# Kernel optimization log

Hardware: AMD Instinct MI355X
Metric: run time of the kernel (lower is better)

## Reference

```python
import jax, jax.numpy as jnp
import numpy as np

B, T, D, L = 16, 4096, 512, 1024

def setup_inputs() -> dict:
    key = jax.random.key(0)
    k1, k2, k3, k4 = jax.random.split(key, 4)
    x = jax.random.normal(k1, (B, T, D), dtype=jnp.float32)
    q = jax.random.normal(k2, (L, D), dtype=jnp.float32)
    fc_w = jax.random.normal(k3, (1, D), dtype=jnp.float32) * (1.0 / np.sqrt(D))
    fc_b = jax.random.normal(k4, (1,), dtype=jnp.float32) * 0.01
    return {"x": x, "q": q, "fc_w": fc_w, "fc_b": fc_b}

def reference(x, q, fc_w, fc_b):
    # att: (B, T, L) label-wise attention scores, softmax over sequence axis T
    att = jnp.einsum('btd,ld->btl', x, q)
    att = jax.nn.softmax(att, axis=1)
    # out: (B, L, D) attention-pooled features per label
    out = jnp.einsum('btl,btd->bld', att, x)
    # linear head to scalar per label -> (B, L)
    return jnp.einsum('bld,od->blo', out, fc_w).squeeze(-1) + fc_b[0]
```

## Files before the change

### kernel.cpp

```cpp
#include <hip/hip_runtime.h>

#define B_ 16
#define T_ 4096
#define D_ 512
#define L_ 1024
#define NTCH (T_ / 64)

typedef _Float16 half8 __attribute__((ext_vector_type(8)));
typedef float float4v __attribute__((ext_vector_type(4)));

__device__ inline void gl_lds(const void* g, void* l) {
    __builtin_amdgcn_global_load_lds(
        (const __attribute__((address_space(1))) unsigned int*)g,
        (__attribute__((address_space(3))) unsigned int*)l, 16, 0, 0);
}

__global__ __launch_bounds__(256) void k_y(const float* __restrict__ x,
                                           const float* __restrict__ w,
                                           float* __restrict__ y) {
    int row  = (blockIdx.x * 256 + threadIdx.x) >> 6;
    int lane = threadIdx.x & 63;
    const float* r = x + (size_t)row * D_;
    float s = 0.f;
#pragma unroll
    for (int k = 0; k < D_; k += 64) s = fmaf(r[k + lane], w[k + lane], s);
#pragma unroll
    for (int o = 32; o > 0; o >>= 1) s += __shfl_xor(s, o, 64);
    if (lane == 0) y[row] = s;
}

__global__ __launch_bounds__(256) void k_cvt(const float* __restrict__ src,
                                             _Float16* __restrict__ dst) {
    int idx = blockIdx.x * 256 + threadIdx.x;
    int g   = idx & 63;
    int row = idx >> 6;
    const float* p = src + (size_t)row * D_ + g * 8;
    float4 a = *(const float4*)p;
    float4 c = *(const float4*)(p + 4);
    half8 h;
    h[0] = (_Float16)a.x; h[1] = (_Float16)a.y; h[2] = (_Float16)a.z; h[3] = (_Float16)a.w;
    h[4] = (_Float16)c.x; h[5] = (_Float16)c.y; h[6] = (_Float16)c.z; h[7] = (_Float16)c.w;
    size_t blk = (size_t)(row >> 4) * (D_ / 32) + (g >> 2);
    ((half8*)dst)[blk * 64 + (row & 15) + 16 * (g & 3)] = h;
}

__global__ __launch_bounds__(256, 2) void k_mfma(const _Float16* __restrict__ xt,
                                                 const _Float16* __restrict__ qt,
                                                 const float* __restrict__ y,
                                                 float* __restrict__ part) {
    __shared__ half8 S[1024];
    __shared__ float ys[128];

    const int tid  = threadIdx.x;
    const int lane = tid & 63;
    const int w    = tid >> 6;
    const int b    = blockIdx.z;
    const int tb0  = b * (T_ / 16) + blockIdx.y * 8;
    const int lb0  = blockIdx.x * 8;

    if (tid < 128) ys[tid] = y[(size_t)b * T_ + blockIdx.y * 128 + tid];

    float4v acc[4][4];
#pragma unroll
    for (int i = 0; i < 4; ++i)
#pragma unroll
        for (int j = 0; j < 4; ++j) acc[i][j] = (float4v){0.f, 0.f, 0.f, 0.f};

    const half8* Xg = (const half8*)xt;
    const half8* Qg = (const half8*)qt;
    const int xa = tb0 + 2 * w;
    const int qa = lb0 + 2 * w;
    const int ts = (w >> 1) * 4, ls = (w & 1) * 4;

    for (int kc = 0; kc < D_ / 32; ++kc) {
        __syncthreads();
        gl_lds(Xg + ((size_t)xa * (D_ / 32) + kc) * 64 + lane,       &S[(2 * w) * 64]);
        gl_lds(Xg + ((size_t)(xa + 1) * (D_ / 32) + kc) * 64 + lane, &S[(2 * w + 1) * 64]);
        gl_lds(Qg + ((size_t)qa * (D_ / 32) + kc) * 64 + lane,       &S[512 + (2 * w) * 64]);
        gl_lds(Qg + ((size_t)(qa + 1) * (D_ / 32) + kc) * 64 + lane, &S[512 + (2 * w + 1) * 64]);
        __syncthreads();

        half8 A[4], Bv[4];
#pragma unroll
        for (int i = 0; i < 4; ++i) A[i] = S[(ts + i) * 64 + lane];
#pragma unroll
        for (int j = 0; j < 4; ++j) Bv[j] = S[512 + (ls + j) * 64 + lane];
#pragma unroll
        for (int i = 0; i < 4; ++i)
#pragma unroll
            for (int j = 0; j < 4; ++j)
                acc[i][j] = __builtin_amdgcn_mfma_f32_16x16x32_f16(A[i], Bv[j], acc[i][j], 0, 0, 0);
    }

    const int quad = lane >> 4, cl = lane & 15;
    const int tw = (w >> 1) * 64;
    const int tchunk = blockIdx.y * 2 + (w >> 1);
    const int lbase = blockIdx.x * 128 + (w & 1) * 64;

#pragma unroll
    for (int j = 0; j < 4; ++j) {
        float m = -1e30f;
#pragma unroll
        for (int i = 0; i < 4; ++i)
#pragma unroll
            for (int r = 0; r < 4; ++r) m = fmaxf(m, acc[i][j][r]);
        float z = 0.f, n = 0.f;
#pragma unroll
        for (int i = 0; i < 4; ++i)
#pragma unroll
            for (int r = 0; r < 4; ++r) {
                float p = __expf(acc[i][j][r] - m);
                z += p;
                n = fmaf(p, ys[tw + i * 16 + quad * 4 + r], n);
            }
#pragma unroll
        for (int msk = 16; msk <= 32; msk <<= 1) {
            float om = __shfl_xor(m, msk, 64);
            float oz = __shfl_xor(z, msk, 64);
            float on = __shfl_xor(n, msk, 64);
            float mn = fmaxf(m, om);
            float s0 = __expf(m - mn), s1 = __expf(om - mn);
            z = fmaf(z, s0, oz * s1);
            n = fmaf(n, s0, on * s1);
            m = mn;
        }
        if (quad == 0) {
            int l = lbase + j * 16 + cl;
            size_t idx = ((size_t)(b * L_ + l) * NTCH + tchunk) * 3;
            part[idx + 0] = m;
            part[idx + 1] = z;
            part[idx + 2] = n;
        }
    }
}

#define NC 8
#define TC (T_ / NC)
#define BT 128
#define BL 128
#define KK 32

__global__ __launch_bounds__(256, 2) void k_main(const float* __restrict__ x,
                                                 const float* __restrict__ q,
                                                 const float* __restrict__ y,
                                                 float* __restrict__ part) {
    __shared__ float Xs[KK][BT + 4];
    __shared__ float Qs[KK][BL + 4];
    const int tid = threadIdx.x;
    const int ty = tid & 15, tx = tid >> 4;
    const int lb = blockIdx.x * BL, chunk = blockIdx.y, b = blockIdx.z;
    const int g = tid & 7, r0 = tid >> 3;

    float run_m[8], run_z[8], run_n[8];
#pragma unroll
    for (int j = 0; j < 8; ++j) { run_m[j] = -1e30f; run_z[j] = 0.f; run_n[j] = 0.f; }

    for (int tt = 0; tt < TC; tt += BT) {
        const int t0 = chunk * TC + tt;
        float s[8][8];
#pragma unroll
        for (int i = 0; i < 8; ++i)
#pragma unroll
            for (int j = 0; j < 8; ++j) s[i][j] = 0.f;
        for (int kc = 0; kc < D_; kc += KK) {
            __syncthreads();
#pragma unroll
            for (int p = 0; p < 4; ++p) {
                int rr = p * 32 + r0;
                float4 vx = *(const float4*)(x + ((size_t)b * T_ + t0 + rr) * D_ + kc + g * 4);
                float4 vq = *(const float4*)(q + (size_t)(lb + rr) * D_ + kc + g * 4);
                Xs[g * 4 + 0][rr] = vx.x; Xs[g * 4 + 1][rr] = vx.y;
                Xs[g * 4 + 2][rr] = vx.z; Xs[g * 4 + 3][rr] = vx.w;
                Qs[g * 4 + 0][rr] = vq.x; Qs[g * 4 + 1][rr] = vq.y;
                Qs[g * 4 + 2][rr] = vq.z; Qs[g * 4 + 3][rr] = vq.w;
            }
            __syncthreads();
#pragma unroll
            for (int k = 0; k < KK; ++k) {
                float4 a0 = *(const float4*)&Xs[k][ty * 4];
                float4 a1 = *(const float4*)&Xs[k][64 + ty * 4];
                float4 b0 = *(const float4*)&Qs[k][tx * 4];
                float4 b1 = *(const float4*)&Qs[k][64 + tx * 4];
                float av[8] = {a0.x, a0.y, a0.z, a0.w, a1.x, a1.y, a1.z, a1.w};
                float bv[8] = {b0.x, b0.y, b0.z, b0.w, b1.x, b1.y, b1.z, b1.w};
#pragma unroll
                for (int i = 0; i < 8; ++i)
#pragma unroll
                    for (int j = 0; j < 8; ++j) s[i][j] = fmaf(av[i], bv[j], s[i][j]);
            }
        }
        float yv[8];
#pragma unroll
        for (int i = 0; i < 8; ++i) {
            int tl = (i < 4) ? (ty * 4 + i) : (64 + ty * 4 + (i - 4));
            yv[i] = y[(size_t)b * T_ + t0 + tl];
        }
#pragma unroll
        for (int j = 0; j < 8; ++j) {
            float mt = s[0][j];
#pragma unroll
            for (int i = 1; i < 8; ++i) mt = fmaxf(mt, s[i][j]);
            float mn = fmaxf(run_m[j], mt);
            float sc = __expf(run_m[j] - mn);
            float z = run_z[j] * sc, n = run_n[j] * sc;
#pragma unroll
            for (int i = 0; i < 8; ++i) {
                float p = __expf(s[i][j] - mn);
                z += p;
                n = fmaf(p, yv[i], n);
            }
            run_m[j] = mn; run_z[j] = z; run_n[j] = n;
        }
    }
#pragma unroll
    for (int msk = 1; msk < 16; msk <<= 1) {
#pragma unroll
        for (int j = 0; j < 8; ++j) {
            float om = __shfl_xor(run_m[j], msk, 64);
            float oz = __shfl_xor(run_z[j], msk, 64);
            float on = __shfl_xor(run_n[j], msk, 64);
            float mn = fmaxf(run_m[j], om);
            float s0 = __expf(run_m[j] - mn), s1 = __expf(om - mn);
            run_z[j] = fmaf(run_z[j], s0, oz * s1);
            run_n[j] = fmaf(run_n[j], s0, on * s1);
            run_m[j] = mn;
        }
    }
    if (ty == 0) {
#pragma unroll
        for (int j = 0; j < 8; ++j) {
            int ll = (j < 4) ? (tx * 4 + j) : (64 + tx * 4 + (j - 4));
            size_t idx = ((size_t)(b * L_ + lb + ll) * NC + chunk) * 3;
            part[idx + 0] = run_m[j];
            part[idx + 1] = run_z[j];
            part[idx + 2] = run_n[j];
        }
    }
}

__global__ __launch_bounds__(256) void k_comb(const float* __restrict__ part,
                                              const float* __restrict__ fc_b,
                                              float* __restrict__ out, int nc) {
    int bl = blockIdx.x * 256 + threadIdx.x;
    float m = -1e30f, z = 0.f, n = 0.f;
    for (int c = 0; c < nc; ++c) {
        size_t idx = ((size_t)bl * nc + c) * 3;
        float pm = part[idx + 0], pz = part[idx + 1], pn = part[idx + 2];
        float mn = fmaxf(m, pm);
        float s0 = __expf(m - mn), s1 = __expf(pm - mn);
        z = fmaf(z, s0, pz * s1);
        n = fmaf(n, s0, pn * s1);
        m = mn;
    }
    out[bl] = n / z + fc_b[0];
}

extern "C" void kernel_launch(void* const* d_in, const int* in_sizes, int n_in,
                              void* d_out, int out_size, void* d_ws, size_t ws_size,
                              hipStream_t stream) {
    const float* x    = (const float*)d_in[0];
    const float* q    = (const float*)d_in[1];
    const float* fc_w = (const float*)d_in[2];
    const float* fc_b = (const float*)d_in[3];
    float* out = (float*)d_out;
    float* ws  = (float*)d_ws;

    const size_t Y_F    = (size_t)B_ * T_;
    const size_t PART_F = (size_t)B_ * L_ * NTCH * 3;
    const size_t XT_H   = (size_t)B_ * T_ * D_;
    const size_t QT_H   = (size_t)L_ * D_;
    const size_t need   = (Y_F + PART_F) * 4 + (XT_H + QT_H) * 2;

    if (ws_size >= need) {
        float* y    = ws;
        float* part = ws + Y_F;
        _Float16* xt = (_Float16*)(ws + Y_F + PART_F);
        _Float16* qt = xt + XT_H;
        k_y  <<<B_ * T_ / 4, 256, 0, stream>>>(x, fc_w, y);
        k_cvt<<<(B_ * T_ * 64) / 256, 256, 0, stream>>>(x, xt);
        k_cvt<<<(L_ * 64) / 256, 256, 0, stream>>>(q, qt);
        k_mfma<<<dim3(L_ / 128, T_ / 128, B_), 256, 0, stream>>>(xt, qt, y, part);
        k_comb<<<B_ * L_ / 256, 256, 0, stream>>>(part, fc_b, out, NTCH);
    } else {
        float* y    = ws;
        float* part = ws + Y_F;
        k_y   <<<B_ * T_ / 4, 256, 0, stream>>>(x, fc_w, y);
        k_main<<<dim3(L_ / BL, NC, B_), 256, 0, stream>>>(x, q, y, part);
        k_comb<<<B_ * L_ / 256, 256, 0, stream>>>(part, fc_b, out, NC);
    }
}
```

Before: 325.4 us.

## Fuse projection and fp16 conversion into one pass; remap MFMA grid for XCD locality

Merges the fc_w projection kernel and the x fp16 conversion into a single k_prep kernel that stages 16 rows in LDS, so x (128 MB fp32) is read from HBM once instead of twice. The MFMA kernel moves to a flat 1D grid whose block index is decoded so consecutive blocks on the same XCD share a (batch, T-tile) and walk the L tiles, improving L2 reuse of the x tile. It also raises launch_bounds occupancy to 4 blocks per CU, which may force register spilling given the 64-float accumulator.

```diff
diff --git a/kernel.cpp b/kernel.cpp
--- a/kernel.cpp
+++ b/kernel.cpp
@@ -27,6 +27,53 @@
 #pragma unroll
     for (int o = 32; o > 0; o >>= 1) s += __shfl_xor(s, o, 64);
     if (lane == 0) y[row] = s;
+}
+
+__global__ __launch_bounds__(256) void k_prep(const float* __restrict__ x,
+                                              const float* __restrict__ w,
+                                              _Float16* __restrict__ xt,
+                                              float* __restrict__ y) {
+    __shared__ float Xl[16 * 512];
+    __shared__ float wl[512];
+    const int tid = threadIdx.x;
+    const size_t base = (size_t)blockIdx.x * (16 * 512);
+
+    if (tid < 128) ((float4*)wl)[tid] = ((const float4*)w)[tid];
+#pragma unroll
+    for (int it = 0; it < 8; ++it) {
+        int f = it * 1024 + tid * 4;
+        ((float4*)Xl)[f >> 2] = *(const float4*)(x + base + f);
+    }
+    __syncthreads();
+
+    {
+        int row = tid >> 4, seg = tid & 15;
+        float p = 0.f;
+#pragma unroll
+        for (int j = 0; j < 32; ++j) {
+            int k = seg * 32 + ((j + tid) & 31);
+            p = fmaf(Xl[row * 512 + k], wl[k], p);
+        }
+        p += __shfl_xor(p, 1, 64); p += __shfl_xor(p, 2, 64);
+        p += __shfl_xor(p, 4, 64); p += __shfl_xor(p, 8, 64);
+        if (seg == 0) y[blockIdx.x * 16 + row] = p;
+    }
+
+    {
+        int idx = tid & 63, row = idx & 15, gq = idx >> 4;
+        half8* dst = (half8*)xt + (size_t)blockIdx.x * (D_ / 32) * 64;
+#pragma unroll
+        for (int it2 = 0; it2 < 4; ++it2) {
+            int kc = it2 * 4 + (tid >> 6);
+            int k0 = kc * 32 + gq * 8;
+            float4 a = *(float4*)&Xl[row * 512 + k0];
+            float4 c = *(float4*)&Xl[row * 512 + k0 + 4];
+            half8 h;
+            h[0] = (_Float16)a.x; h[1] = (_Float16)a.y; h[2] = (_Float16)a.z; h[3] = (_Float16)a.w;
+            h[4] = (_Float16)c.x; h[5] = (_Float16)c.y; h[6] = (_Float16)c.z; h[7] = (_Float16)c.w;
+            dst[kc * 64 + idx] = h;
+        }
+    }
 }
 
 __global__ __launch_bounds__(256) void k_cvt(const float* __restrict__ src,
@@ -44,21 +91,28 @@
     ((half8*)dst)[blk * 64 + (row & 15) + 16 * (g & 3)] = h;
 }
 
-__global__ __launch_bounds__(256, 2) void k_mfma(const _Float16* __restrict__ xt,
+__global__ __launch_bounds__(256, 4) void k_mfma(const _Float16* __restrict__ xt,
                                                  const _Float16* __restrict__ qt,
                                                  const float* __restrict__ y,
                                                  float* __restrict__ part) {
     __shared__ half8 S[1024];
     __shared__ float ys[128];
 
+    const int bid  = blockIdx.x;
+    const int xcd  = bid & 7;
+    const int jj   = bid >> 3;
+    const int tile = (xcd << 6) | (jj >> 3);
+    const int lblk = jj & 7;
+    const int tblk = tile & 31;
+    const int b    = tile >> 5;
+
     const int tid  = threadIdx.x;
     const int lane = tid & 63;
     const int w    = tid >> 6;
-    const int b    = blockIdx.z;
-    const int tb0  = b * (T_ / 16) + blockIdx.y * 8;
-    const int lb0  = blockIdx.x * 8;
-
-    if (tid < 128) ys[tid] = y[(size_t)b * T_ + blockIdx.y * 128 + tid];
+    const int tb0  = b * (T_ / 16) + tblk * 8;
+    const int lb0  = lblk * 8;
+
+    if (tid < 128) ys[tid] = y[(size_t)b * T_ + tblk * 128 + tid];
 
     float4v acc[4][4];
 #pragma unroll
@@ -94,8 +148,8 @@
 
     const int quad = lane >> 4, cl = lane & 15;
     const int tw = (w >> 1) * 64;
-    const int tchunk = blockIdx.y * 2 + (w >> 1);
-    const int lbase = blockIdx.x * 128 + (w & 1) * 64;
+    const int tchunk = tblk * 2 + (w >> 1);
+    const int lbase = lblk * 128 + (w & 1) * 64;
 
 #pragma unroll
     for (int j = 0; j < 4; ++j) {
@@ -276,10 +330,9 @@
         float* part = ws + Y_F;
         _Float16* xt = (_Float16*)(ws + Y_F + PART_F);
         _Float16* qt = xt + XT_H;
-        k_y  <<<B_ * T_ / 4, 256, 0, stream>>>(x, fc_w, y);
-        k_cvt<<<(B_ * T_ * 64) / 256, 256, 0, stream>>>(x, xt);
-        k_cvt<<<(L_ * 64) / 256, 256, 0, stream>>>(q, qt);
-        k_mfma<<<dim3(L_ / 128, T_ / 128, B_), 256, 0, stream>>>(xt, qt, y, part);
+        k_prep<<<B_ * T_ / 16, 256, 0, stream>>>(x, fc_w, xt, y);
+        k_cvt <<<(L_ * 64) / 256, 256, 0, stream>>>(q, qt);
+        k_mfma<<<4096, 256, 0, stream>>>(xt, qt, y, part);
         k_comb<<<B_ * L_ / 256, 256, 0, stream>>>(part, fc_b, out, NTCH);
     } else {
         float* y    = ws;
```

Result: faster. 301.5 us (-7.3%).

## Fuse fp16 conversion with fc dot-product, remap MFMA grid per XCD, planar partials

Applied to the files above, without the earlier changes.

Merges the separate y = x·fc_w reduction and the fp16 layout conversion into one prep kernel, so x is read once instead of twice. The MFMA kernel moves to a 1D grid with an XCD-aware block mapping that keeps tiles of the same batch on the same XCD to improve L2 reuse, and its launch-bounds occupancy hint rises from 2 to 4. Partial softmax stats are stored as separate planes indexed by L contiguously, so the combine kernel reads coalesced. Occupancy 4 may force register spills given 64 accumulator floats per thread.

```diff
diff --git a/kernel.cpp b/kernel.cpp
--- a/kernel.cpp
+++ b/kernel.cpp
@@ -5,6 +5,7 @@
 #define D_ 512
 #define L_ 1024
 #define NTCH (T_ / 64)
+#define PPLANE ((size_t)B_ * NTCH * L_)
 
 typedef _Float16 half8 __attribute__((ext_vector_type(8)));
 typedef float float4v __attribute__((ext_vector_type(4)));
@@ -15,50 +16,70 @@
         (__attribute__((address_space(3))) unsigned int*)l, 16, 0, 0);
 }
 
-__global__ __launch_bounds__(256) void k_y(const float* __restrict__ x,
-                                           const float* __restrict__ w,
-                                           float* __restrict__ y) {
-    int row  = (blockIdx.x * 256 + threadIdx.x) >> 6;
-    int lane = threadIdx.x & 63;
-    const float* r = x + (size_t)row * D_;
-    float s = 0.f;
-#pragma unroll
-    for (int k = 0; k < D_; k += 64) s = fmaf(r[k + lane], w[k + lane], s);
-#pragma unroll
-    for (int o = 32; o > 0; o >>= 1) s += __shfl_xor(s, o, 64);
-    if (lane == 0) y[row] = s;
-}
-
-__global__ __launch_bounds__(256) void k_cvt(const float* __restrict__ src,
-                                             _Float16* __restrict__ dst) {
-    int idx = blockIdx.x * 256 + threadIdx.x;
-    int g   = idx & 63;
-    int row = idx >> 6;
-    const float* p = src + (size_t)row * D_ + g * 8;
-    float4 a = *(const float4*)p;
-    float4 c = *(const float4*)(p + 4);
-    half8 h;
-    h[0] = (_Float16)a.x; h[1] = (_Float16)a.y; h[2] = (_Float16)a.z; h[3] = (_Float16)a.w;
-    h[4] = (_Float16)c.x; h[5] = (_Float16)c.y; h[6] = (_Float16)c.z; h[7] = (_Float16)c.w;
-    size_t blk = (size_t)(row >> 4) * (D_ / 32) + (g >> 2);
-    ((half8*)dst)[blk * 64 + (row & 15) + 16 * (g & 3)] = h;
-}
-
-__global__ __launch_bounds__(256, 2) void k_mfma(const _Float16* __restrict__ xt,
+__global__ __launch_bounds__(256) void k_prep(const float* __restrict__ src,
+                                              const float* __restrict__ w,
+                                              _Float16* __restrict__ dst,
+                                              float* __restrict__ y, int do_y) {
+    __shared__ float Yp[64];
+    const int tid  = threadIdx.x;
+    const int wv   = tid >> 6;
+    const int lane = tid & 63;
+    const int row  = lane & 15, gq = lane >> 4;
+    const float* bsrc = src + (size_t)blockIdx.x * (16 * 512);
+    half8* bdst = (half8*)dst + (size_t)blockIdx.x * 1024;
+
+    float acc = 0.f;
+#pragma unroll
+    for (int it = 0; it < 4; ++it) {
+        int kc = it * 4 + wv;
+        int k0 = kc * 32 + gq * 8;
+        float4 a = *(const float4*)(bsrc + row * 512 + k0);
+        float4 c = *(const float4*)(bsrc + row * 512 + k0 + 4);
+        half8 h;
+        h[0] = (_Float16)a.x; h[1] = (_Float16)a.y; h[2] = (_Float16)a.z; h[3] = (_Float16)a.w;
+        h[4] = (_Float16)c.x; h[5] = (_Float16)c.y; h[6] = (_Float16)c.z; h[7] = (_Float16)c.w;
+        bdst[kc * 64 + lane] = h;
+        if (do_y) {
+            float4 wa = *(const float4*)(w + k0);
+            float4 wc = *(const float4*)(w + k0 + 4);
+            acc = fmaf(a.x, wa.x, acc); acc = fmaf(a.y, wa.y, acc);
+            acc = fmaf(a.z, wa.z, acc); acc = fmaf(a.w, wa.w, acc);
+            acc = fmaf(c.x, wc.x, acc); acc = fmaf(c.y, wc.y, acc);
+            acc = fmaf(c.z, wc.z, acc); acc = fmaf(c.w, wc.w, acc);
+        }
+    }
+    if (do_y) {
+        acc += __shfl_xor(acc, 16, 64);
+        acc += __shfl_xor(acc, 32, 64);
+        if (gq == 0) Yp[wv * 16 + row] = acc;
+        __syncthreads();
+        if (tid < 16)
+            y[blockIdx.x * 16 + tid] = Yp[tid] + Yp[16 + tid] + Yp[32 + tid] + Yp[48 + tid];
+    }
+}
+
+__global__ __launch_bounds__(256, 4) void k_mfma(const _Float16* __restrict__ xt,
                                                  const _Float16* __restrict__ qt,
                                                  const float* __restrict__ y,
                                                  float* __restrict__ part) {
     __shared__ half8 S[1024];
     __shared__ float ys[128];
 
+    const int bid  = blockIdx.x;
+    const int xcd  = bid & 7;
+    const int jj   = bid >> 3;
+    const int tile = (xcd << 6) | (jj >> 3);
+    const int lblk = jj & 7;
+    const int tblk = tile & 31;
+    const int b    = tile >> 5;
+
     const int tid  = threadIdx.x;
     const int lane = tid & 63;
     const int w    = tid >> 6;
-    const int b    = blockIdx.z;
-    const int tb0  = b * (T_ / 16) + blockIdx.y * 8;
-    const int lb0  = blockIdx.x * 8;
-
-    if (tid < 128) ys[tid] = y[(size_t)b * T_ + blockIdx.y * 128 + tid];
+    const int tb0  = b * (T_ / 16) + tblk * 8;
+    const int lb0  = lblk * 8;
+
+    if (tid < 128) ys[tid] = y[(size_t)b * T_ + tblk * 128 + tid];
 
     float4v acc[4][4];
 #pragma unroll
@@ -94,8 +115,12 @@
 
     const int quad = lane >> 4, cl = lane & 15;
     const int tw = (w >> 1) * 64;
-    const int tchunk = blockIdx.y * 2 + (w >> 1);
-    const int lbase = blockIdx.x * 128 + (w & 1) * 64;
+    const int tchunk = tblk * 2 + (w >> 1);
+    const int lbase = lblk * 128 + (w & 1) * 64;
+
+    float* pm = part;
+    float* pz = part + PPLANE;
+    float* pn = part + 2 * PPLANE;
 
 #pragma unroll
     for (int j = 0; j < 4; ++j) {
@@ -126,12 +151,33 @@
         }
         if (quad == 0) {
             int l = lbase + j * 16 + cl;
-            size_t idx = ((size_t)(b * L_ + l) * NTCH + tchunk) * 3;
-            part[idx + 0] = m;
-            part[idx + 1] = z;
-            part[idx + 2] = n;
-        }
-    }
+            size_t a = ((size_t)b * NTCH + tchunk) * L_ + l;
+            pm[a] = m;
+            pz[a] = z;
+            pn[a] = n;
+        }
+    }
+}
+
+__global__ __launch_bounds__(256) void k_comb_p(const float* __restrict__ part,
+                                                const float* __restrict__ fc_b,
+                                                float* __restrict__ out) {
+    int bl = blockIdx.x * 256 + threadIdx.x;
+    int b = bl >> 10, l = bl & (L_ - 1);
+    const float* pm = part;
+    const float* pz = part + PPLANE;
+    const float* pn = part + 2 * PPLANE;
+    float m = -1e30f, z = 0.f, n = 0.f;
+    for (int c = 0; c < NTCH; ++c) {
+        size_t a = ((size_t)b * NTCH + c) * L_ + l;
+        float pmv = pm[a], pzv = pz[a], pnv = pn[a];
+        float mn = fmaxf(m, pmv);
+        float s0 = __expf(m - mn), s1 = __expf(pmv - mn);
+        z = fmaf(z, s0, pzv * s1);
+        n = fmaf(n, s0, pnv * s1);
+        m = mn;
+    }
+    out[bl] = n / z + fc_b[0];
 }
 
 #define NC 8
@@ -139,6 +185,20 @@
 #define BT 128
 #define BL 128
 #define KK 32
+
+__global__ __launch_bounds__(256) void k_y(const float* __restrict__ x,
+                                           const float* __restrict__ w,
+                                           float* __restrict__ y) {
+    int row  = (blockIdx.x * 256 + threadIdx.x) >> 6;
+    int lane = threadIdx.x & 63;
+    const float* r = x + (size_t)row * D_;
+    float s = 0.f;
+#pragma unroll
+    for (int k = 0; k < D_; k += 64) s = fmaf(r[k + lane], w[k + lane], s);
+#pragma unroll
+    for (int o = 32; o > 0; o >>= 1) s += __shfl_xor(s, o, 64);
+    if (lane == 0) y[row] = s;
+}
 
 __global__ __launch_bounds__(256, 2) void k_main(const float* __restrict__ x,
                                                  const float* __restrict__ q,
@@ -238,13 +298,13 @@
     }
 }
 
-__global__ __launch_bounds__(256) void k_comb(const float* __restrict__ part,
-                                              const float* __restrict__ fc_b,
-                                              float* __restrict__ out, int nc) {
+__global__ __launch_bounds__(256) void k_comb_f(const float* __restrict__ part,
+                                                const float* __restrict__ fc_b,
+                                                float* __restrict__ out) {
     int bl = blockIdx.x * 256 + threadIdx.x;
     float m = -1e30f, z = 0.f, n = 0.f;
-    for (int c = 0; c < nc; ++c) {
-        size_t idx = ((size_t)bl * nc + c) * 3;
+    for (int c = 0; c < NC; ++c) {
+        size_t idx = ((size_t)bl * NC + c) * 3;
         float pm = part[idx + 0], pz = part[idx + 1], pn = part[idx + 2];
         float mn = fmaxf(m, pm);
         float s0 = __expf(m - mn), s1 = __expf(pm - mn);
@@ -266,7 +326,7 @@
     float* ws  = (float*)d_ws;
 
     const size_t Y_F    = (size_t)B_ * T_;
-    const size_t PART_F = (size_t)B_ * L_ * NTCH * 3;
+    const size_t PART_F = 3 * PPLANE;
     const size_t XT_H   = (size_t)B_ * T_ * D_;
     const size_t QT_H   = (size_t)L_ * D_;
     const size_t need   = (Y_F + PART_F) * 4 + (XT_H + QT_H) * 2;
@@ -276,16 +336,15 @@
         float* part = ws + Y_F;
         _Float16* xt = (_Float16*)(ws + Y_F + PART_F);
         _Float16* qt = xt + XT_H;
-        k_y  <<<B_ * T_ / 4, 256, 0, stream>>>(x, fc_w, y);
-        k_cvt<<<(B_ * T_ * 64) / 256, 256, 0, stream>>>(x, xt);
-        k_cvt<<<(L_ * 64) / 256, 256, 0, stream>>>(q, qt);
-        k_mfma<<<dim3(L_ / 128, T_ / 128, B_), 256, 0, stream>>>(xt, qt, y, part);
-        k_comb<<<B_ * L_ / 256, 256, 0, stream>>>(part, fc_b, out, NTCH);
+        k_prep<<<B_ * T_ / 16, 256, 0, stream>>>(x, fc_w, xt, y, 1);
+        k_prep<<<L_ / 16, 256, 0, stream>>>(q, fc_w, qt, nullptr, 0);
+        k_mfma<<<4096, 256, 0, stream>>>(xt, qt, y, part);
+        k_comb_p<<<B_ * L_ / 256, 256, 0, stream>>>(part, fc_b, out);
     } else {
         float* y    = ws;
         float* part = ws + Y_F;
         k_y   <<<B_ * T_ / 4, 256, 0, stream>>>(x, fc_w, y);
         k_main<<<dim3(L_ / BL, NC, B_), 256, 0, stream>>>(x, q, y, part);
-        k_comb<<<B_ * L_ / 256, 256, 0, stream>>>(part, fc_b, out, NC);
-    }
-}
+        k_comb_f<<<B_ * L_ / 256, 256, 0, stream>>>(part, fc_b, out);
+    }
+}
```

Result: faster. 290.6 us (-10.7%).
